# Optimization experiments

Hardware: AMD Instinct MI355X
Metric: run time of the kernel (lower is better)

The kernel has to match this reference:

```python
import jax, jax.numpy as jnp
import numpy as np

N, E, B, C, L, HLS = 30000, 480000, 64, 128, 3, 64
PARAM_NAMES = ['Wq','bq','Wk','bk','Wv','bv','Wskip','bskip','lstm_Wih_f','lstm_Whh_f','lstm_bih_f','lstm_bhh_f','lstm_Wih_b','lstm_Whh_b','lstm_bih_b','lstm_bhh_b','att_W','att_b','gP_W1','gP_b1','gP_W2','gP_b2','gT_W1','gT_b1','gT_W2','gT_b2','m_W0','m_b0','m_W1','m_b1','m_W2','m_b2']


def setup_inputs() -> dict:
    key = jax.random.key(0)
    ks = iter(jax.random.split(key, 64))
    rn = lambda shape: jax.random.normal(next(ks), shape, dtype=jnp.float32) * 0.05
    inp = {
        'x': jax.random.normal(next(ks), (N, C), dtype=jnp.float32),
        'edge_index': jax.random.randint(next(ks), (2, E), 0, N, dtype=jnp.int32),
        'batch': jnp.sort(jax.random.randint(next(ks), (N,), 0, B, dtype=jnp.int32)),
        'hls_attr': jax.random.normal(next(ks), (B, HLS), dtype=jnp.float32),
        'Wq': rn((L, C, C)), 'bq': rn((L, C)),
        'Wk': rn((L, C, C)), 'bk': rn((L, C)),
        'Wv': rn((L, C, C)), 'bv': rn((L, C)),
        'Wskip': rn((L, C, C)), 'bskip': rn((L, C)),
        'lstm_Wih_f': rn((4 * C, C)), 'lstm_Whh_f': rn((4 * C, C)),
        'lstm_bih_f': rn((4 * C,)), 'lstm_bhh_f': rn((4 * C,)),
        'lstm_Wih_b': rn((4 * C, C)), 'lstm_Whh_b': rn((4 * C, C)),
        'lstm_bih_b': rn((4 * C,)), 'lstm_bhh_b': rn((4 * C,)),
        'att_W': rn((2 * C, 1)), 'att_b': rn((1,)),
        'gP_W1': rn((C, C)), 'gP_b1': rn((C,)), 'gP_W2': rn((C, 1)), 'gP_b2': rn((1,)),
        'gT_W1': rn((C, C)), 'gT_b1': rn((C,)), 'gT_W2': rn((C, 1)), 'gT_b2': rn((1,)),
        'm_W0': rn((2 * C + HLS, 64)), 'm_b0': rn((64,)),
        'm_W1': rn((64, 64)), 'm_b1': rn((64,)),
        'm_W2': rn((64, 1)), 'm_b2': rn((1,)),
    }
    return inp


def _segment_softmax(logits, seg, num):
    m = jax.ops.segment_max(logits, seg, num_segments=num)
    e = jnp.exp(logits - m[seg])
    d = jax.ops.segment_sum(e, seg, num_segments=num)
    return e / d[seg]


def _lstm(xs, Wih, Whh, bih, bhh):
    # xs: [L, N, C] -> outputs [L, N, H]
    H = Whh.shape[1]
    h0 = jnp.zeros((xs.shape[1], H), xs.dtype)
    bias = bih + bhh
    def step(carry, xt):
        h, c = carry
        z = xt @ Wih.T + h @ Whh.T + bias
        i, f, g, o = jnp.split(z, 4, axis=-1)
        c = jax.nn.sigmoid(f) * c + jax.nn.sigmoid(i) * jnp.tanh(g)
        h = jax.nn.sigmoid(o) * jnp.tanh(c)
        return (h, c), h
    _, hs = jax.lax.scan(step, (h0, h0), xs)
    return hs


def _gate_pool(x, batch, W1, b1, W2, b2):
    gate = jax.nn.relu(x @ W1 + b1) @ W2 + b2          # [N, 1]
    gate = _segment_softmax(gate[:, 0], batch, B)[:, None]
    return jax.ops.segment_sum(gate * x, batch, num_segments=B)


def _forward(x, edge_index, batch, hls_attr, Wq, bq, Wk, bk, Wv, bv, Wskip, bskip,
             lstm_Wih_f, lstm_Whh_f, lstm_bih_f, lstm_bhh_f,
             lstm_Wih_b, lstm_Whh_b, lstm_bih_b, lstm_bhh_b,
             att_W, att_b, gP_W1, gP_b1, gP_W2, gP_b2, gT_W1, gT_b1, gT_W2, gT_b2,
             m_W0, m_b0, m_W1, m_b1, m_W2, m_b2):
    src, dst = edge_index[0], edge_index[1]
    scale = 1.0 / jnp.sqrt(jnp.asarray(C, jnp.float32))
    h_list = []
    for i in range(L):
        q = x @ Wq[i] + bq[i]
        k = x @ Wk[i] + bk[i]
        v = x @ Wv[i] + bv[i]
        logits = jnp.sum(q[dst] * k[src], axis=-1) * scale   # [E]
        alpha = _segment_softmax(logits, dst, N)             # per-dst softmax
        agg = jax.ops.segment_sum(alpha[:, None] * v[src], dst, num_segments=N)
        x = jax.nn.relu(agg + x @ Wskip[i] + bskip[i])       # TransformerConv + root skip, then ReLU
        h_list.append(x)
    xs = jnp.stack(h_list)                                   # [L, N, C]
    hf = _lstm(xs, lstm_Wih_f, lstm_Whh_f, lstm_bih_f, lstm_bhh_f)
    hb = _lstm(xs[::-1], lstm_Wih_b, lstm_Whh_b, lstm_bih_b, lstm_bhh_b)[::-1]
    hcat = jnp.concatenate([hf, hb], axis=-1)                # [L, N, 2C]
    a = jax.nn.softmax((hcat @ att_W)[..., 0] + att_b[0], axis=0)  # softmax over layers
    x = jnp.sum(a[..., None] * xs, axis=0)                   # [N, C] JK-LSTM output
    out_P = _gate_pool(x, batch, gP_W1, gP_b1, gP_W2, gP_b2)
    out_T = _gate_pool(x, batch, gT_W1, gT_b1, gT_W2, gT_b2)
    h = jnp.concatenate([out_P, out_T, hls_attr], axis=-1)   # [B, 2C+HLS]
    h = jax.nn.relu(h @ m_W0 + m_b0)
    h = jax.nn.relu(h @ m_W1 + m_b1)
    return h @ m_W2 + m_b2                                   # [B, 1]


def reference(x, edge_index, batch, hls_attr, Wq, bq, Wk, bk, Wv, bv, Wskip, bskip,
              lstm_Wih_f, lstm_Whh_f, lstm_bih_f, lstm_bhh_f,
              lstm_Wih_b, lstm_Whh_b, lstm_bih_b, lstm_bhh_b,
              att_W, att_b, gP_W1, gP_b1, gP_W2, gP_b2, gT_W1, gT_b1, gT_W2, gT_b2,
              m_W0, m_b0, m_W1, m_b1, m_W2, m_b2):
    return _forward(x, edge_index, batch, hls_attr, Wq, bq, Wk, bk, Wv, bv, Wskip, bskip,
                    lstm_Wih_f, lstm_Whh_f, lstm_bih_f, lstm_bhh_f,
                    lstm_Wih_b, lstm_Whh_b, lstm_bih_b, lstm_bhh_b,
                    att_W, att_b, gP_W1, gP_b1, gP_W2, gP_b2, gT_W1, gT_b1, gT_W2, gT_b2,
                    m_W0, m_b0, m_W1, m_b1, m_W2, m_b2)
```

## Files before the change

### kernel.cpp

```cpp
#include <hip/hip_runtime.h>
#include <math.h>

#define NN 30000
#define EE 480000
#define BB 64
#define CC 128
#define LLAYERS 3
#define HLSD 64

typedef __attribute__((ext_vector_type(8))) short bf16x8;
typedef __attribute__((ext_vector_type(4))) float f32x4;
typedef unsigned short u16;

__device__ inline unsigned short f2bf(float f){
  unsigned u = __float_as_uint(f);
  u += 0x7fffu + ((u >> 16) & 1u);
  return (unsigned short)(u >> 16);
}
__device__ inline float bf2f(unsigned short h){
  return __uint_as_float(((unsigned)h) << 16);
}
__device__ inline float fsig(float z){
  return __builtin_amdgcn_rcpf(1.f + __expf(-z));
}
__device__ inline float ftanh(float z){
  return 1.f - 2.f*__builtin_amdgcn_rcpf(1.f + __expf(2.f*z));
}

__global__ void k_hist(const int* __restrict__ dst, int* __restrict__ counts, int E){
  int e = blockIdx.x*256 + threadIdx.x;
  if (e < E) atomicAdd(&counts[dst[e]], 1);
}
__global__ void k_scan_block(const int* __restrict__ counts, int* __restrict__ row_ptr,
                             int* __restrict__ bsums, int n){
  __shared__ int sm[256];
  int i = blockIdx.x*256 + threadIdx.x;
  int v = (i < n) ? counts[i] : 0;
  sm[threadIdx.x] = v; __syncthreads();
  for (int off = 1; off < 256; off <<= 1){
    int t = (threadIdx.x >= off) ? sm[threadIdx.x - off] : 0;
    __syncthreads();
    sm[threadIdx.x] += t;
    __syncthreads();
  }
  if (i < n) row_ptr[i+1] = sm[threadIdx.x];
  if (threadIdx.x == 255) bsums[blockIdx.x] = sm[255];
}
__global__ void k_scan_bsums(const int* __restrict__ bsums, int* __restrict__ bexcl, int nb){
  if (threadIdx.x == 0 && blockIdx.x == 0){
    int s = 0;
    for (int i = 0; i < nb; i++){ int t = bsums[i]; bexcl[i] = s; s += t; }
  }
}
__global__ void k_scan_add(int* __restrict__ row_ptr, const int* __restrict__ bexcl, int n){
  int i = blockIdx.x*256 + threadIdx.x;
  if (i < n) row_ptr[i+1] += bexcl[i >> 8];
  if (i == 0) row_ptr[0] = 0;
}
__global__ void k_fill(const int* __restrict__ src, const int* __restrict__ dst,
                       const int* __restrict__ row_ptr, int* __restrict__ fill,
                       int* __restrict__ esrc, int E){
  int e = blockIdx.x*256 + threadIdx.x;
  if (e < E){
    int d = dst[e];
    int pos = row_ptr[d] + atomicAdd(&fill[d], 1);
    esrc[pos] = src[e];
  }
}

struct PrepPtrs {
  const float* tsrc[14]; unsigned short* tdst[14];
  const float* csrc[4];  unsigned short* cdst[4];
  const float *bihf, *bhhf, *bihb, *bhhb;
  float *cbf, *cbb;
};
__global__ __launch_bounds__(256) void k_prep(PrepPtrs p){
  int b = blockIdx.x, tid = threadIdx.x;
  if (b < 14){
    const float* s = p.tsrc[b]; unsigned short* d = p.tdst[b];
    for (int i = tid; i < 16384; i += 256){
      int k = i >> 7, n = i & 127;
      d[n*128 + k] = f2bf(s[i]);
    }
  } else if (b < 30){
    int m = (b - 14) >> 2, ch = (b - 14) & 3;
    const float* s = p.csrc[m] + ch*16384; unsigned short* d = p.cdst[m] + ch*16384;
    for (int i = tid; i < 16384; i += 256) d[i] = f2bf(s[i]);
  } else {
    for (int i = tid; i < 512; i += 256){
      p.cbf[i] = p.bihf[i] + p.bhhf[i];
      p.cbb[i] = p.bihb[i] + p.bhhb[i];
    }
  }
}
__global__ __launch_bounds__(256) void k_cvt_x(const float* __restrict__ src,
                                               unsigned short* __restrict__ dst, int n8){
  int i = blockIdx.x*256 + threadIdx.x;
  if (i >= n8) return;
  float4 a = *(const float4*)(src + (size_t)i*8);
  float4 b = *(const float4*)(src + (size_t)i*8 + 4);
  union { unsigned short u[8]; uint4 v; } o;
  o.u[0]=f2bf(a.x); o.u[1]=f2bf(a.y); o.u[2]=f2bf(a.z); o.u[3]=f2bf(a.w);
  o.u[4]=f2bf(b.x); o.u[5]=f2bf(b.y); o.u[6]=f2bf(b.z); o.u[7]=f2bf(b.w);
  *(uint4*)(dst + (size_t)i*8) = o.v;
}

struct Quad { const unsigned short* Bt[4]; const float* bias[4]; };

template<int RELU, int OUTBF16>
__global__ __launch_bounds__(256) void k_mfma_gemm(
    const unsigned short* __restrict__ A0, Quad qd,
    float* __restrict__ Cf, unsigned short* __restrict__ Cb,
    int M, int ldC, int colsPerMat)
{
  __shared__ unsigned short As0[64*128];
  __shared__ unsigned short Bs0[64*128];

  const int tid = threadIdx.x;
  const int row0 = blockIdx.x*64;
  const int colg0 = blockIdx.y*64;
  const int mi = colg0 / colsPerMat;
  const int nloc = colg0 - mi*colsPerMat;
  const unsigned short* Bt0 = qd.Bt[mi];

  #pragma unroll
  for (int i = 0; i < 4; i++){
    int ch = tid + i*256;
    int r = ch >> 4, c16 = ch & 15;
    int gr = row0 + r;
    uint4 av = make_uint4(0,0,0,0);
    if (gr < M) av = *(const uint4*)(A0 + (size_t)gr*128 + c16*8);
    *(uint4*)((char*)As0 + ((r*256 + c16*16) ^ ((r&7)<<4))) = av;
    uint4 bv = *(const uint4*)(Bt0 + (size_t)(nloc + r)*128 + c16*8);
    *(uint4*)((char*)Bs0 + ((r*256 + c16*16) ^ ((r&7)<<4))) = bv;
  }
  __syncthreads();

  const int w = tid >> 6, l = tid & 63;
  const int lr = l & 15, lhi = l >> 4;

  f32x4 acc[4];
  #pragma unroll
  for (int f = 0; f < 4; f++){ acc[f][0]=0.f; acc[f][1]=0.f; acc[f][2]=0.f; acc[f][3]=0.f; }

  #pragma unroll
  for (int kt = 0; kt < 4; kt++){
    int arow = w*16 + lr;
    bf16x8 a = *(const bf16x8*)((const char*)As0 + ((arow*256 + kt*64 + lhi*16) ^ ((arow&7)<<4)));
    #pragma unroll
    for (int f = 0; f < 4; f++){
      int brow = f*16 + lr;
      bf16x8 b = *(const bf16x8*)((const char*)Bs0 + ((brow*256 + kt*64 + lhi*16) ^ ((brow&7)<<4)));
      acc[f] = __builtin_amdgcn_mfma_f32_16x16x32_bf16(a, b, acc[f], 0, 0, 0);
    }
  }

  const float* bias = qd.bias[mi];
  #pragma unroll
  for (int f = 0; f < 4; f++){
    int colg = colg0 + f*16 + lr;
    float bv = bias ? bias[nloc + f*16 + lr] : 0.f;
    #pragma unroll
    for (int r = 0; r < 4; r++){
      int grow = row0 + w*16 + lhi*4 + r;
      if (grow < M){
        float v = acc[f][r] + bv;
        if (RELU) v = fmaxf(v, 0.f);
        if (OUTBF16) Cb[(size_t)grow*ldC + colg] = f2bf(v);
        else         Cf[(size_t)grow*ldC + colg] = v;
      }
    }
  }
}

struct LstmArgs {
  const u16 *Xf, *Xb, *Hf, *Hb;
  const u16 *Wihf, *Whhf, *Wihb, *Whhb;
  const float *cbf, *cbb;
  u16 *Hof, *Hob;
  float *Cf, *Cb2;
  float *scF, *scB;
  const float* attW;
  int M;
};
template<int FIRST>
__global__ __launch_bounds__(256) void k_lstm2(LstmArgs a){
  __shared__ unsigned short As[64*128];
  __shared__ unsigned short Bs[128*128];
  const int dir = blockIdx.y >> 2;
  const int t0 = (blockIdx.y & 3)*32;
  const u16* X = dir ? a.Xb : a.Xf;
  const u16* H = dir ? a.Hb : a.Hf;
  const u16* Wih = dir ? a.Wihb : a.Wihf;
  const u16* Whh = dir ? a.Whhb : a.Whhf;
  const float* cbias = dir ? a.cbb : a.cbf;
  u16* Hout = dir ? a.Hob : a.Hof;
  float* Cst = dir ? a.Cb2 : a.Cf;
  float* score = dir ? a.scB : a.scF;
  const float* attW = a.attW + dir*128;
  const int M = a.M;

  const int tid = threadIdx.x;
  const int row0 = blockIdx.x*64;
  const int w = tid >> 6, l = tid & 63, lr = l & 15, lhi = l >> 4;

  f32x4 acc[8];
  #pragma unroll
  for (int f = 0; f < 8; f++){ acc[f][0]=0.f; acc[f][1]=0.f; acc[f][2]=0.f; acc[f][3]=0.f; }

  const int npair = FIRST ? 1 : 2;
  for (int pair = 0; pair < npair; pair++){
    const unsigned short* A  = pair ? H   : X;
    const unsigned short* Bt = pair ? Whh : Wih;
    if (pair) __syncthreads();
    #pragma unroll
    for (int i = 0; i < 4; i++){
      int ch = tid + i*256;
      int r = ch >> 4, c16 = ch & 15;
      int gr = row0 + r;
      uint4 av = make_uint4(0,0,0,0);
      if (gr < M) av = *(const uint4*)(A + (size_t)gr*128 + c16*8);
      *(uint4*)((char*)As + ((r*256 + c16*16) ^ ((r&7)<<4))) = av;
    }
    #pragma unroll
    for (int i = 0; i < 8; i++){
      int ch = tid + i*256;
      int r = ch >> 4, c16 = ch & 15;
      int gr = (r >> 5)*128 + t0 + (r & 31);
      uint4 bv = *(const uint4*)(Bt + (size_t)gr*128 + c16*8);
      *(uint4*)((char*)Bs + ((r*256 + c16*16) ^ ((r&7)<<4))) = bv;
    }
    __syncthreads();
    #pragma unroll
    for (int kt = 0; kt < 4; kt++){
      int arow = w*16 + lr;
      bf16x8 av = *(const bf16x8*)((const char*)As + ((arow*256 + kt*64 + lhi*16) ^ ((arow&7)<<4)));
      #pragma unroll
      for (int f = 0; f < 8; f++){
        int brow = f*16 + lr;
        bf16x8 bv = *(const bf16x8*)((const char*)Bs + ((brow*256 + kt*64 + lhi*16) ^ ((brow&7)<<4)));
        acc[f] = __builtin_amdgcn_mfma_f32_16x16x32_bf16(av, bv, acc[f], 0, 0, 0);
      }
    }
  }

  float sc[4] = {0.f, 0.f, 0.f, 0.f};
  #pragma unroll
  for (int cb = 0; cb < 2; cb++){
    int t = t0 + cb*16 + lr;
    float aw  = attW[t];
    float bi  = cbias[t];
    float bf_ = cbias[128 + t];
    float bg  = cbias[256 + t];
    float bo  = cbias[384 + t];
    #pragma unroll
    for (int r = 0; r < 4; r++){
      int grow = row0 + w*16 + lhi*4 + r;
      if (grow < M){
        float zi = acc[0+cb][r] + bi;
        float zf = acc[2+cb][r] + bf_;
        float zg = acc[4+cb][r] + bg;
        float zo = acc[6+cb][r] + bo;
        float cp = FIRST ? 0.f : Cst[(size_t)grow*128 + t];
        float cn = fsig(zf)*cp + fsig(zi)*ftanh(zg);
        float hn = fsig(zo)*ftanh(cn);
        Cst[(size_t)grow*128 + t] = cn;
        Hout[(size_t)grow*128 + t] = f2bf(hn);
        sc[r] += hn * aw;
      }
    }
  }
  #pragma unroll
  for (int r = 0; r < 4; r++){
    float p = sc[r];
    p += __shfl_xor(p, 1, 64);
    p += __shfl_xor(p, 2, 64);
    p += __shfl_xor(p, 4, 64);
    p += __shfl_xor(p, 8, 64);
    if (lr == 0){
      int grow = row0 + w*16 + lhi*4 + r;
      if (grow < M) atomicAdd(&score[grow], p);
    }
  }
}

__global__ __launch_bounds__(256) void k_attn(
    const unsigned short* __restrict__ qkvs, const int* __restrict__ row_ptr,
    const int* __restrict__ esrc, unsigned short* __restrict__ xout, int n)
{
  int wid = threadIdx.x >> 6, lane = threadIdx.x & 63;
  int dst = blockIdx.x*4 + wid;
  if (dst >= n) return;
  const int g = lane >> 4, j = lane & 15;
  const size_t drow = (size_t)dst*512;

  bf16x8 qv = *(const bf16x8*)(qkvs + drow + j*8);
  float qf[8];
  #pragma unroll
  for (int i = 0; i < 8; i++) qf[i] = bf2f((unsigned short)qv[i]);

  const int rs = row_ptr[dst], re = row_ptr[dst+1];
  const float scale2 = 0.08838834764831845f * 1.4426950408889634f;
  float m = -INFINITY, den = 0.f;
  float acc[8];
  #pragma unroll
  for (int i = 0; i < 8; i++) acc[i] = 0.f;

  int e = rs + g;
  if (e < re){
    int s = esrc[e];
    const unsigned short* sr = qkvs + (size_t)s*512 + j*8;
    bf16x8 kc = *(const bf16x8*)(sr + 128);
    bf16x8 vc = *(const bf16x8*)(sr + 256);
    while (true){
      int en = e + 4;
      bool havenext = en < re;
      bf16x8 kn, vn;
      if (havenext){
        int sn = esrc[en];
        const unsigned short* srn = qkvs + (size_t)sn*512 + j*8;
        kn = *(const bf16x8*)(srn + 128);
        vn = *(const bf16x8*)(srn + 256);
      }
      float d = qf[0]*bf2f((unsigned short)kc[0]);
      #pragma unroll
      for (int i = 1; i < 8; i++) d += qf[i]*bf2f((unsigned short)kc[i]);
      d += __shfl_xor(d, 1, 64);
      d += __shfl_xor(d, 2, 64);
      d += __shfl_xor(d, 4, 64);
      d += __shfl_xor(d, 8, 64);
      float logit = d * scale2;
      float mn = fmaxf(m, logit);
      float rr = exp2f(m - mn);
      float wgt = exp2f(logit - mn);
      den = den*rr + wgt;
      #pragma unroll
      for (int i = 0; i < 8; i++)
        acc[i] = acc[i]*rr + wgt*bf2f((unsigned short)vc[i]);
      m = mn;
      if (!havenext) break;
      e = en; kc = kn; vc = vn;
    }
  }

  #pragma unroll
  for (int o = 16; o <= 32; o <<= 1){
    float mo  = __shfl_xor(m, o, 64);
    float dno = __shfl_xor(den, o, 64);
    float mn  = fmaxf(m, mo);
    float ss  = (m  > -INFINITY) ? exp2f(m  - mn) : 0.f;
    float so  = (mo > -INFINITY) ? exp2f(mo - mn) : 0.f;
    den = den*ss + dno*so;
    #pragma unroll
    for (int i = 0; i < 8; i++){
      float ao = __shfl_xor(acc[i], o, 64);
      acc[i] = acc[i]*ss + ao*so;
    }
    m = mn;
  }

  if (g == 0){
    bf16x8 sk = *(const bf16x8*)(qkvs + drow + 384 + j*8);
    float inv = (re > rs) ? 1.f/den : 0.f;
    union { unsigned short u[8]; uint4 v; } o8;
    #pragma unroll
    for (int i = 0; i < 8; i++){
      float v = acc[i]*inv + bf2f((unsigned short)sk[i]);
      o8.u[i] = f2bf(fmaxf(v, 0.f));
    }
    *(uint4*)(xout + (size_t)dst*128 + j*8) = o8.v;
  }
}

__global__ void k_jk_weights(const float* __restrict__ sF, const float* __restrict__ sB,
                             const float* __restrict__ attb, float* __restrict__ a, int n){
  int i = blockIdx.x*256 + threadIdx.x;
  if (i >= n) return;
  float s0 = sF[i]       + sB[i]       + attb[0];
  float s1 = sF[n+i]     + sB[n+i]     + attb[0];
  float s2 = sF[2*n+i]   + sB[2*n+i]   + attb[0];
  float mm = fmaxf(s0, fmaxf(s1, s2));
  float e0 = __expf(s0-mm), e1 = __expf(s1-mm), e2 = __expf(s2-mm);
  float d = e0 + e1 + e2;
  a[i] = e0/d; a[n+i] = e1/d; a[2*n+i] = e2/d;
}
__global__ void k_jk_combine(const float* __restrict__ a,
                             const unsigned short* __restrict__ x0,
                             const unsigned short* __restrict__ x1,
                             const unsigned short* __restrict__ x2,
                             float* __restrict__ xjk, unsigned short* __restrict__ xjkb, int n){
  int i8 = blockIdx.x*256 + threadIdx.x;
  if (i8 >= n*16) return;
  int node = i8 >> 4;
  float a0 = a[node], a1 = a[n+node], a2 = a[2*n+node];
  bf16x8 v0 = *(const bf16x8*)(x0 + (size_t)i8*8);
  bf16x8 v1 = *(const bf16x8*)(x1 + (size_t)i8*8);
  bf16x8 v2 = *(const bf16x8*)(x2 + (size_t)i8*8);
  float r[8];
  union { unsigned short u[8]; uint4 v; } ob;
  #pragma unroll
  for (int i = 0; i < 8; i++){
    r[i] = a0*bf2f((unsigned short)v0[i]) + a1*bf2f((unsigned short)v1[i]) + a2*bf2f((unsigned short)v2[i]);
    ob.u[i] = f2bf(r[i]);
  }
  float4* xo = (float4*)(xjk + (size_t)i8*8);
  xo[0] = make_float4(r[0], r[1], r[2], r[3]);
  xo[1] = make_float4(r[4], r[5], r[6], r[7]);
  *(uint4*)(xjkb + (size_t)i8*8) = ob.v;
}

__global__ __launch_bounds__(256) void k_rowdot2(
    const unsigned short* __restrict__ g,
    const float* __restrict__ w2P, const float* __restrict__ w2T,
    const float* __restrict__ b2P, const float* __restrict__ b2T,
    float* __restrict__ glP, float* __restrict__ glT, int n)
{
  int wid = threadIdx.x >> 6, lane = threadIdx.x & 63;
  int node = blockIdx.x*4 + wid;
  if (node >= n) return;
  ushort4 gv = *(const ushort4*)(g + (size_t)node*256 + lane*4);
  const float* w = (lane >= 32) ? w2T : w2P;
  int c0 = (lane*4) & 127;
  float4 wv = *(const float4*)(w + c0);
  float p = bf2f(gv.x)*wv.x + bf2f(gv.y)*wv.y + bf2f(gv.z)*wv.z + bf2f(gv.w)*wv.w;
  #pragma unroll
  for (int o = 1; o < 32; o <<= 1) p += __shfl_xor(p, o, 64);
  if (lane == 0)  glP[node] = p + b2P[0];
  if (lane == 32) glT[node] = p + b2T[0];
}

__global__ void k_segbounds(const int* __restrict__ batch, int* __restrict__ segp, int n){
  int i = blockIdx.x*256 + threadIdx.x;
  if (i >= n) return;
  int b = batch[i];
  int bp = (i == 0) ? -1 : batch[i-1];
  for (int s = bp+1; s <= b; s++) segp[s] = i;
  if (i == n-1){
    for (int s = b+1; s <= BB; s++) segp[s] = n;
  }
}

__global__ __launch_bounds__(256) void k_seg_stats(
    const float* __restrict__ glP, const float* __restrict__ glT,
    const int* __restrict__ segp, float4* __restrict__ stats)
{
  const int b = blockIdx.x, tid = threadIdx.x;
  const int s0 = segp[b], s1 = segp[b+1];
  __shared__ float sred[8];

  float mP = -INFINITY, mT = -INFINITY;
  for (int i = s0 + tid; i < s1; i += 256){
    mP = fmaxf(mP, glP[i]);
    mT = fmaxf(mT, glT[i]);
  }
  #pragma unroll
  for (int o = 1; o < 64; o <<= 1){
    mP = fmaxf(mP, __shfl_xor(mP, o, 64));
    mT = fmaxf(mT, __shfl_xor(mT, o, 64));
  }
  if ((tid & 63) == 0){ sred[(tid >> 6)*2] = mP; sred[(tid >> 6)*2 + 1] = mT; }
  __syncthreads();
  mP = fmaxf(fmaxf(sred[0], sred[2]), fmaxf(sred[4], sred[6]));
  mT = fmaxf(fmaxf(sred[1], sred[3]), fmaxf(sred[5], sred[7]));
  __syncthreads();

  float dP = 0.f, dT = 0.f;
  for (int i = s0 + tid; i < s1; i += 256){
    dP += __expf(glP[i] - mP);
    dT += __expf(glT[i] - mT);
  }
  #pragma unroll
  for (int o = 1; o < 64; o <<= 1){
    dP += __shfl_xor(dP, o, 64);
    dT += __shfl_xor(dT, o, 64);
  }
  if ((tid & 63) == 0){ sred[(tid >> 6)*2] = dP; sred[(tid >> 6)*2 + 1] = dT; }
  __syncthreads();
  if (tid == 0){
    dP = sred[0] + sred[2] + sred[4] + sred[6];
    dT = sred[1] + sred[3] + sred[5] + sred[7];
    float4 st;
    st.x = mP; st.y = mT;
    st.z = (dP > 0.f) ? 1.f/dP : 0.f;
    st.w = (dT > 0.f) ? 1.f/dT : 0.f;
    stats[b] = st;
  }
}

__global__ __launch_bounds__(256) void k_poolsum(
    const float* __restrict__ xjk, const int* __restrict__ segp,
    const float* __restrict__ glP, const float* __restrict__ glT,
    const float4* __restrict__ stats,
    float* __restrict__ poolP, float* __restrict__ poolT)
{
  const int b = blockIdx.x;
  const int s0 = segp[b], s1 = segp[b+1];
  const float4 st = stats[b];
  const int half = threadIdx.x >> 7, c = threadIdx.x & 127;
  const int stream = blockIdx.y*2 + half;
  float aP = 0.f, aT = 0.f;
  for (int i = s0 + stream; i < s1; i += 32){
    float eP = __expf(glP[i] - st.x);
    float eT = __expf(glT[i] - st.y);
    float xv = xjk[(size_t)i*128 + c];
    aP += eP*xv; aT += eT*xv;
  }
  if (aP != 0.f) atomicAdd(&poolP[(size_t)b*128 + c], aP*st.z);
  if (aT != 0.f) atomicAdd(&poolT[(size_t)b*128 + c], aT*st.w);
}

__global__ __launch_bounds__(64) void k_mlp(
    const float* __restrict__ poolP, const float* __restrict__ poolT, const float* __restrict__ hls,
    const float* __restrict__ W0, const float* __restrict__ b0,
    const float* __restrict__ W1, const float* __restrict__ b1,
    const float* __restrict__ W2, const float* __restrict__ b2, float* __restrict__ out)
{
  __shared__ float hin[320];
  __shared__ float h1[64];
  int b = blockIdx.x, j = threadIdx.x;
  for (int i = j; i < 320; i += 64){
    float vv;
    if (i < 128)      vv = poolP[(size_t)b*128 + i];
    else if (i < 256) vv = poolT[(size_t)b*128 + (i-128)];
    else              vv = hls[(size_t)b*64 + (i-256)];
    hin[i] = vv;
  }
  __syncthreads();
  float s = b0[j];
  for (int kk = 0; kk < 320; kk++) s += hin[kk] * W0[kk*64 + j];
  h1[j] = fmaxf(s, 0.f);
  __syncthreads();
  float s2 = b1[j];
  for (int kk = 0; kk < 64; kk++) s2 += h1[kk] * W1[kk*64 + j];
  float h2 = fmaxf(s2, 0.f);
  float p = h2 * W2[j];
  #pragma unroll
  for (int o = 1; o < 64; o <<= 1) p += __shfl_xor(p, o, 64);
  if (j == 0) out[b] = p + b2[0];
}

extern "C" void kernel_launch(void* const* d_in, const int* in_sizes, int n_in,
                              void* d_out, int out_size, void* d_ws, size_t ws_size,
                              hipStream_t stream)
{
  (void)in_sizes; (void)n_in; (void)out_size; (void)ws_size;
  const int N = NN, E = EE, C = CC;
  const float* x     = (const float*)d_in[0];
  const int*   ei    = (const int*)d_in[1];
  const int*   batch = (const int*)d_in[2];
  const float* hls   = (const float*)d_in[3];
  const float* Wq = (const float*)d_in[4],  *bq = (const float*)d_in[5];
  const float* Wk = (const float*)d_in[6],  *bk = (const float*)d_in[7];
  const float* Wv = (const float*)d_in[8],  *bv = (const float*)d_in[9];
  const float* Ws = (const float*)d_in[10], *bs = (const float*)d_in[11];
  const float* Wih_f = (const float*)d_in[12], *Whh_f = (const float*)d_in[13];
  const float* bih_f = (const float*)d_in[14], *bhh_f = (const float*)d_in[15];
  const float* Wih_b = (const float*)d_in[16], *Whh_b = (const float*)d_in[17];
  const float* bih_b = (const float*)d_in[18], *bhh_b = (const float*)d_in[19];
  const float* attW  = (const float*)d_in[20], *attb  = (const float*)d_in[21];
  const float* gPW1 = (const float*)d_in[22], *gPb1 = (const float*)d_in[23];
  const float* gPW2 = (const float*)d_in[24], *gPb2 = (const float*)d_in[25];
  const float* gTW1 = (const float*)d_in[26], *gTb1 = (const float*)d_in[27];
  const float* gTW2 = (const float*)d_in[28], *gTb2 = (const float*)d_in[29];
  const float* mW0 = (const float*)d_in[30], *mb0 = (const float*)d_in[31];
  const float* mW1 = (const float*)d_in[32], *mb1 = (const float*)d_in[33];
  const float* mW2 = (const float*)d_in[34], *mb2 = (const float*)d_in[35];
  float* out = (float*)d_out;

  const int* esrc_in = ei;
  const int* edst_in = ei + E;

  char* ws = (char*)d_ws;
  size_t off = 0;
  auto alloc = [&](size_t bytes) -> char* {
    char* p = ws + off;
    off += (bytes + 255) & ~(size_t)255;
    return p;
  };
  u16* qkvsb   = (u16*)alloc((size_t)N*512*2);
  u16* xb      = (u16*)alloc((size_t)N*C*2);
  u16* xsb0    = (u16*)alloc((size_t)N*C*2);
  u16* xsb1    = (u16*)alloc((size_t)N*C*2);
  u16* xsb2    = (u16*)alloc((size_t)N*C*2);
  u16* hfA     = (u16*)alloc((size_t)N*C*2);
  u16* hfB     = (u16*)alloc((size_t)N*C*2);
  u16* hbA     = (u16*)alloc((size_t)N*C*2);
  u16* hbB     = (u16*)alloc((size_t)N*C*2);
  float* cfb   = (float*)alloc((size_t)N*C*4);
  float* cbb2  = (float*)alloc((size_t)N*C*4);
  float* scores= (float*)alloc((size_t)6*N*4);
  float* ajk   = (float*)alloc((size_t)3*N*4);
  float* xjk   = (float*)alloc((size_t)N*C*4);
  u16* xjkb    = (u16*)alloc((size_t)N*C*2);
  u16* g1PT    = (u16*)alloc((size_t)N*256*2);
  int* counts  = (int*)alloc((size_t)N*4);
  int* row_ptr = (int*)alloc((size_t)(N+1)*4);
  int* bsums   = (int*)alloc(512);
  int* bexcl   = (int*)alloc(512);
  int* esrc    = (int*)alloc((size_t)E*4);
  float* glP   = (float*)alloc((size_t)N*4);
  float* glT   = (float*)alloc((size_t)N*4);
  int* segp    = (int*)alloc((size_t)(BB+1)*4);
  float* poolP = (float*)alloc((size_t)BB*C*4);
  float* poolT = (float*)alloc((size_t)BB*C*4);
  float4* sstats = (float4*)alloc((size_t)BB*16);
  u16* wT      = (u16*)alloc((size_t)14*16384*2);
  u16* wLSTM   = (u16*)alloc((size_t)4*65536*2);
  float* combF = (float*)alloc(512*4);
  float* combB = (float*)alloc(512*4);

  float* scF = scores;
  float* scB = scores + (size_t)3*N;

  u16* wTq = wT;
  u16* wTk = wT + 3*16384;
  u16* wTv = wT + 6*16384;
  u16* wTs = wT + 9*16384;
  u16* wTgP = wT + 12*16384;
  u16* wTgT = wT + 13*16384;
  u16* wIHf = wLSTM;
  u16* wHHf = wLSTM + 65536;
  u16* wIHb = wLSTM + 2*65536;
  u16* wHHb = wLSTM + 3*65536;

  const int NB  = (N + 255)/256;
  const int EBL = (E + 255)/256;

  PrepPtrs pp;
  for (int l = 0; l < 3; l++){
    pp.tsrc[l]   = Wq + (size_t)l*16384;  pp.tdst[l]   = wTq + (size_t)l*16384;
    pp.tsrc[3+l] = Wk + (size_t)l*16384;  pp.tdst[3+l] = wTk + (size_t)l*16384;
    pp.tsrc[6+l] = Wv + (size_t)l*16384;  pp.tdst[6+l] = wTv + (size_t)l*16384;
    pp.tsrc[9+l] = Ws + (size_t)l*16384;  pp.tdst[9+l] = wTs + (size_t)l*16384;
  }
  pp.tsrc[12] = gPW1; pp.tdst[12] = wTgP;
  pp.tsrc[13] = gTW1; pp.tdst[13] = wTgT;
  pp.csrc[0] = Wih_f; pp.cdst[0] = wIHf;
  pp.csrc[1] = Whh_f; pp.cdst[1] = wHHf;
  pp.csrc[2] = Wih_b; pp.cdst[2] = wIHb;
  pp.csrc[3] = Whh_b; pp.cdst[3] = wHHb;
  pp.bihf = bih_f; pp.bhhf = bhh_f; pp.bihb = bih_b; pp.bhhb = bhh_b;
  pp.cbf = combF; pp.cbb = combB;
  k_prep<<<31, 256, 0, stream>>>(pp);
  k_cvt_x<<<(N*C/8 + 255)/256, 256, 0, stream>>>(x, xb, N*C/8);

  hipMemsetAsync(counts, 0, (size_t)N*4, stream);
  k_hist<<<EBL, 256, 0, stream>>>(edst_in, counts, E);
  k_scan_block<<<NB, 256, 0, stream>>>(counts, row_ptr, bsums, N);
  k_scan_bsums<<<1, 64, 0, stream>>>(bsums, bexcl, NB);
  k_scan_add<<<NB, 256, 0, stream>>>(row_ptr, bexcl, N);
  hipMemsetAsync(counts, 0, (size_t)N*4, stream);
  k_fill<<<EBL, 256, 0, stream>>>(esrc_in, edst_in, row_ptr, counts, esrc, E);

  const int GX = (N + 63)/64;
  dim3 blk(256);

  u16* xsb[3] = {xsb0, xsb1, xsb2};
  const u16* ain = xb;
  for (int l = 0; l < LLAYERS; l++){
    Quad q;
    q.Bt[0] = wTq + (size_t)l*16384;  q.bias[0] = bq + (size_t)l*C;
    q.Bt[1] = wTk + (size_t)l*16384;  q.bias[1] = bk + (size_t)l*C;
    q.Bt[2] = wTv + (size_t)l*16384;  q.bias[2] = bv + (size_t)l*C;
    q.Bt[3] = wTs + (size_t)l*16384;  q.bias[3] = bs + (size_t)l*C;
    k_mfma_gemm<0,1><<<dim3(GX,8), blk, 0, stream>>>(ain, q, nullptr, qkvsb, N, 512, 128);
    k_attn<<<(N+3)/4, 256, 0, stream>>>(qkvsb, row_ptr, esrc, xsb[l], N);
    ain = xsb[l];
  }

  hipMemsetAsync(scores, 0, (size_t)6*N*4, stream);
  {
    u16* hfbuf[2] = {hfA, hfB};
    u16* hbbuf[2] = {hbA, hbB};
    for (int step = 0; step < 3; step++){
      LstmArgs la;
      la.Xf = xsb[step]; la.Xb = xsb[2-step];
      la.Hf = hfbuf[(step&1)^1]; la.Hb = hbbuf[(step&1)^1];
      la.Wihf = wIHf; la.Whhf = wHHf; la.Wihb = wIHb; la.Whhb = wHHb;
      la.cbf = combF; la.cbb = combB;
      la.Hof = hfbuf[step&1]; la.Hob = hbbuf[step&1];
      la.Cf = cfb; la.Cb2 = cbb2;
      la.scF = scF + (size_t)step*N; la.scB = scB + (size_t)(2-step)*N;
      la.attW = attW; la.M = N;
      if (step == 0) k_lstm2<1><<<dim3(GX,8), blk, 0, stream>>>(la);
      else           k_lstm2<0><<<dim3(GX,8), blk, 0, stream>>>(la);
    }
  }

  k_jk_weights<<<NB, 256, 0, stream>>>(scF, scB, attb, ajk, N);
  k_jk_combine<<<(N*16 + 255)/256, 256, 0, stream>>>(ajk, xsb0, xsb1, xsb2, xjk, xjkb, N);

  {
    Quad qg;
    qg.Bt[0] = wTgP; qg.bias[0] = gPb1;
    qg.Bt[1] = wTgT; qg.bias[1] = gTb1;
    qg.Bt[2] = nullptr; qg.bias[2] = nullptr;
    qg.Bt[3] = nullptr; qg.bias[3] = nullptr;
    k_mfma_gemm<1,1><<<dim3(GX,4), blk, 0, stream>>>(xjkb, qg, nullptr, g1PT, N, 256, 128);
    k_rowdot2<<<(N+3)/4, 256, 0, stream>>>(g1PT, gPW2, gTW2, gPb2, gTb2, glP, glT, N);
  }

  k_segbounds<<<NB, 256, 0, stream>>>(batch, segp, N);
  k_seg_stats<<<BB, 256, 0, stream>>>(glP, glT, segp, sstats);
  hipMemsetAsync(poolP, 0, (size_t)2*BB*C*4, stream);
  k_poolsum<<<dim3(BB,16), 256, 0, stream>>>(xjk, segp, glP, glT, sstats, poolP, poolT);

  k_mlp<<<BB, 64, 0, stream>>>(poolP, poolT, hls, mW0, mb0, mW1, mb1, mW2, mb2, out);
}
```

Before: 472.3 us.

## Fuse three bidirectional LSTM steps into one kernel with on-chip h/c state

The three per-step LSTM launches are replaced by a single kernel. Each block owns 64 rows and one direction, and it loops over all three timesteps and all four gate strips. Hidden state stays in LDS and cell state in registers, so the global H/C buffers, the score memset and the atomics are removed. In exchange, the grid shrinks from 8 to 2 blocks in y, which lowers parallelism. Weight tiles are also reloaded per strip per step with more syncs, and LDS use rises to about 80KB, which limits occupancy.

```diff
diff --git a/kernel.cpp b/kernel.cpp
--- a/kernel.cpp
+++ b/kernel.cpp
@@ -173,114 +173,147 @@
   }
 }
 
-struct LstmArgs {
-  const u16 *Xf, *Xb, *Hf, *Hb;
-  const u16 *Wihf, *Whhf, *Wihb, *Whhb;
-  const float *cbf, *cbb;
-  u16 *Hof, *Hob;
-  float *Cf, *Cb2;
-  float *scF, *scB;
-  const float* attW;
-  int M;
-};
-template<int FIRST>
-__global__ __launch_bounds__(256) void k_lstm2(LstmArgs a){
-  __shared__ unsigned short As[64*128];
-  __shared__ unsigned short Bs[128*128];
-  const int dir = blockIdx.y >> 2;
-  const int t0 = (blockIdx.y & 3)*32;
-  const u16* X = dir ? a.Xb : a.Xf;
-  const u16* H = dir ? a.Hb : a.Hf;
-  const u16* Wih = dir ? a.Wihb : a.Wihf;
-  const u16* Whh = dir ? a.Whhb : a.Whhf;
-  const float* cbias = dir ? a.cbb : a.cbf;
-  u16* Hout = dir ? a.Hob : a.Hof;
-  float* Cst = dir ? a.Cb2 : a.Cf;
-  float* score = dir ? a.scB : a.scF;
-  const float* attW = a.attW + dir*128;
-  const int M = a.M;
+__global__ __launch_bounds__(256) void k_lstm_all(
+    const u16* __restrict__ xsA, const u16* __restrict__ xsB, const u16* __restrict__ xsC,
+    const u16* __restrict__ WihF, const u16* __restrict__ WhhF,
+    const u16* __restrict__ WihB, const u16* __restrict__ WhhB,
+    const float* __restrict__ cbF, const float* __restrict__ cbB,
+    const float* __restrict__ attWall,
+    float* __restrict__ scF, float* __restrict__ scB, int M)
+{
+  __shared__ u16 Xs[64*128];
+  __shared__ u16 Hs[2][64*128];
+  __shared__ u16 Bs[128*128];
+
+  const int dir = blockIdx.y;
+  const u16* Wih = dir ? WihB : WihF;
+  const u16* Whh = dir ? WhhB : WhhF;
+  const float* cbias = dir ? cbB : cbF;
+  const float* attW = attWall + dir*128;
+  float* score = dir ? scB : scF;
+  const u16* xsrc[3];
+  xsrc[0] = dir ? xsC : xsA;
+  xsrc[1] = xsB;
+  xsrc[2] = dir ? xsA : xsC;
 
   const int tid = threadIdx.x;
   const int row0 = blockIdx.x*64;
   const int w = tid >> 6, l = tid & 63, lr = l & 15, lhi = l >> 4;
-
-  f32x4 acc[8];
-  #pragma unroll
-  for (int f = 0; f < 8; f++){ acc[f][0]=0.f; acc[f][1]=0.f; acc[f][2]=0.f; acc[f][3]=0.f; }
-
-  const int npair = FIRST ? 1 : 2;
-  for (int pair = 0; pair < npair; pair++){
-    const unsigned short* A  = pair ? H   : X;
-    const unsigned short* Bt = pair ? Whh : Wih;
-    if (pair) __syncthreads();
+  const int lrowbase = w*16 + lhi*4;
+
+  float cst[4][8];
+  #pragma unroll
+  for (int s = 0; s < 4; s++)
+    #pragma unroll
+    for (int i = 0; i < 8; i++) cst[s][i] = 0.f;
+
+  int cur = 0;
+  for (int t = 0; t < 3; t++){
+    const u16* X = xsrc[t];
+    __syncthreads();
     #pragma unroll
     for (int i = 0; i < 4; i++){
       int ch = tid + i*256;
       int r = ch >> 4, c16 = ch & 15;
       int gr = row0 + r;
       uint4 av = make_uint4(0,0,0,0);
-      if (gr < M) av = *(const uint4*)(A + (size_t)gr*128 + c16*8);
-      *(uint4*)((char*)As + ((r*256 + c16*16) ^ ((r&7)<<4))) = av;
-    }
+      if (gr < M) av = *(const uint4*)(X + (size_t)gr*128 + c16*8);
+      *(uint4*)((char*)Xs + ((r*256 + c16*16) ^ ((r&7)<<4))) = av;
+    }
+    u16* hwr = Hs[cur ^ 1];
+    const u16* hrd = Hs[cur];
+    float scacc[4] = {0.f, 0.f, 0.f, 0.f};
+
     #pragma unroll
-    for (int i = 0; i < 8; i++){
-      int ch = tid + i*256;
-      int r = ch >> 4, c16 = ch & 15;
-      int gr = (r >> 5)*128 + t0 + (r & 31);
-      uint4 bv = *(const uint4*)(Bt + (size_t)gr*128 + c16*8);
-      *(uint4*)((char*)Bs + ((r*256 + c16*16) ^ ((r&7)<<4))) = bv;
-    }
-    __syncthreads();
-    #pragma unroll
-    for (int kt = 0; kt < 4; kt++){
-      int arow = w*16 + lr;
-      bf16x8 av = *(const bf16x8*)((const char*)As + ((arow*256 + kt*64 + lhi*16) ^ ((arow&7)<<4)));
+    for (int strip = 0; strip < 4; strip++){
+      const int t0 = strip*32;
+      f32x4 acc[8];
       #pragma unroll
-      for (int f = 0; f < 8; f++){
-        int brow = f*16 + lr;
-        bf16x8 bv = *(const bf16x8*)((const char*)Bs + ((brow*256 + kt*64 + lhi*16) ^ ((brow&7)<<4)));
-        acc[f] = __builtin_amdgcn_mfma_f32_16x16x32_bf16(av, bv, acc[f], 0, 0, 0);
+      for (int f = 0; f < 8; f++){ acc[f][0]=0.f; acc[f][1]=0.f; acc[f][2]=0.f; acc[f][3]=0.f; }
+
+      #pragma unroll
+      for (int i = 0; i < 8; i++){
+        int ch = tid + i*256;
+        int r = ch >> 4, c16 = ch & 15;
+        int gr = (r >> 5)*128 + t0 + (r & 31);
+        uint4 bv = *(const uint4*)(Wih + (size_t)gr*128 + c16*8);
+        *(uint4*)((char*)Bs + ((r*256 + c16*16) ^ ((r&7)<<4))) = bv;
       }
-    }
-  }
-
-  float sc[4] = {0.f, 0.f, 0.f, 0.f};
-  #pragma unroll
-  for (int cb = 0; cb < 2; cb++){
-    int t = t0 + cb*16 + lr;
-    float aw  = attW[t];
-    float bi  = cbias[t];
-    float bf_ = cbias[128 + t];
-    float bg  = cbias[256 + t];
-    float bo  = cbias[384 + t];
+      __syncthreads();
+      #pragma unroll
+      for (int kt = 0; kt < 4; kt++){
+        int arow = w*16 + lr;
+        bf16x8 av = *(const bf16x8*)((const char*)Xs + ((arow*256 + kt*64 + lhi*16) ^ ((arow&7)<<4)));
+        #pragma unroll
+        for (int f = 0; f < 8; f++){
+          int brow = f*16 + lr;
+          bf16x8 bv = *(const bf16x8*)((const char*)Bs + ((brow*256 + kt*64 + lhi*16) ^ ((brow&7)<<4)));
+          acc[f] = __builtin_amdgcn_mfma_f32_16x16x32_bf16(av, bv, acc[f], 0, 0, 0);
+        }
+      }
+      if (t > 0){
+        __syncthreads();
+        #pragma unroll
+        for (int i = 0; i < 8; i++){
+          int ch = tid + i*256;
+          int r = ch >> 4, c16 = ch & 15;
+          int gr = (r >> 5)*128 + t0 + (r & 31);
+          uint4 bv = *(const uint4*)(Whh + (size_t)gr*128 + c16*8);
+          *(uint4*)((char*)Bs + ((r*256 + c16*16) ^ ((r&7)<<4))) = bv;
+        }
+        __syncthreads();
+        #pragma unroll
+        for (int kt = 0; kt < 4; kt++){
+          int arow = w*16 + lr;
+          bf16x8 av = *(const bf16x8*)((const char*)hrd + ((arow*256 + kt*64 + lhi*16) ^ ((arow&7)<<4)));
+          #pragma unroll
+          for (int f = 0; f < 8; f++){
+            int brow = f*16 + lr;
+            bf16x8 bv = *(const bf16x8*)((const char*)Bs + ((brow*256 + kt*64 + lhi*16) ^ ((brow&7)<<4)));
+            acc[f] = __builtin_amdgcn_mfma_f32_16x16x32_bf16(av, bv, acc[f], 0, 0, 0);
+          }
+        }
+      }
+      #pragma unroll
+      for (int cb = 0; cb < 2; cb++){
+        int ch = t0 + cb*16 + lr;
+        float aw  = attW[ch];
+        float bi  = cbias[ch];
+        float bf_ = cbias[128 + ch];
+        float bg  = cbias[256 + ch];
+        float bo  = cbias[384 + ch];
+        #pragma unroll
+        for (int r = 0; r < 4; r++){
+          float zi = acc[0+cb][r] + bi;
+          float zf = acc[2+cb][r] + bf_;
+          float zg = acc[4+cb][r] + bg;
+          float zo = acc[6+cb][r] + bo;
+          float cp = cst[strip][cb*4+r];
+          float cn = fsig(zf)*cp + fsig(zi)*ftanh(zg);
+          float hn = fsig(zo)*ftanh(cn);
+          cst[strip][cb*4+r] = cn;
+          int lrow = lrowbase + r;
+          *(u16*)((char*)hwr + ((lrow*256 + ch*2) ^ ((lrow&7)<<4))) = f2bf(hn);
+          scacc[r] += hn * aw;
+        }
+      }
+      __syncthreads();
+    }
+
+    const int soff = (dir ? (2 - t) : t) * M;
     #pragma unroll
     for (int r = 0; r < 4; r++){
-      int grow = row0 + w*16 + lhi*4 + r;
-      if (grow < M){
-        float zi = acc[0+cb][r] + bi;
-        float zf = acc[2+cb][r] + bf_;
-        float zg = acc[4+cb][r] + bg;
-        float zo = acc[6+cb][r] + bo;
-        float cp = FIRST ? 0.f : Cst[(size_t)grow*128 + t];
-        float cn = fsig(zf)*cp + fsig(zi)*ftanh(zg);
-        float hn = fsig(zo)*ftanh(cn);
-        Cst[(size_t)grow*128 + t] = cn;
-        Hout[(size_t)grow*128 + t] = f2bf(hn);
-        sc[r] += hn * aw;
+      float p = scacc[r];
+      p += __shfl_xor(p, 1, 64);
+      p += __shfl_xor(p, 2, 64);
+      p += __shfl_xor(p, 4, 64);
+      p += __shfl_xor(p, 8, 64);
+      if (lr == 0){
+        int grow = row0 + lrowbase + r;
+        if (grow < M) score[soff + grow] = p;
       }
     }
-  }
-  #pragma unroll
-  for (int r = 0; r < 4; r++){
-    float p = sc[r];
-    p += __shfl_xor(p, 1, 64);
-    p += __shfl_xor(p, 2, 64);
-    p += __shfl_xor(p, 4, 64);
-    p += __shfl_xor(p, 8, 64);
-    if (lr == 0){
-      int grow = row0 + w*16 + lhi*4 + r;
-      if (grow < M) atomicAdd(&score[grow], p);
-    }
+    cur ^= 1;
   }
 }
 
@@ -582,12 +615,6 @@
   u16* xsb0    = (u16*)alloc((size_t)N*C*2);
   u16* xsb1    = (u16*)alloc((size_t)N*C*2);
   u16* xsb2    = (u16*)alloc((size_t)N*C*2);
-  u16* hfA     = (u16*)alloc((size_t)N*C*2);
-  u16* hfB     = (u16*)alloc((size_t)N*C*2);
-  u16* hbA     = (u16*)alloc((size_t)N*C*2);
-  u16* hbB     = (u16*)alloc((size_t)N*C*2);
-  float* cfb   = (float*)alloc((size_t)N*C*4);
-  float* cbb2  = (float*)alloc((size_t)N*C*4);
   float* scores= (float*)alloc((size_t)6*N*4);
   float* ajk   = (float*)alloc((size_t)3*N*4);
   float* xjk   = (float*)alloc((size_t)N*C*4);
@@ -668,24 +695,8 @@
     ain = xsb[l];
   }
 
-  hipMemsetAsync(scores, 0, (size_t)6*N*4, stream);
-  {
-    u16* hfbuf[2] = {hfA, hfB};
-    u16* hbbuf[2] = {hbA, hbB};
-    for (int step = 0; step < 3; step++){
-      LstmArgs la;
-      la.Xf = xsb[step]; la.Xb = xsb[2-step];
-      la.Hf = hfbuf[(step&1)^1]; la.Hb = hbbuf[(step&1)^1];
-      la.Wihf = wIHf; la.Whhf = wHHf; la.Wihb = wIHb; la.Whhb = wHHb;
-      la.cbf = combF; la.cbb = combB;
-      la.Hof = hfbuf[step&1]; la.Hob = hbbuf[step&1];
-      la.Cf = cfb; la.Cb2 = cbb2;
-      la.scF = scF + (size_t)step*N; la.scB = scB + (size_t)(2-step)*N;
-      la.attW = attW; la.M = N;
-      if (step == 0) k_lstm2<1><<<dim3(GX,8), blk, 0, stream>>>(la);
-      else           k_lstm2<0><<<dim3(GX,8), blk, 0, stream>>>(la);
-    }
-  }
+  k_lstm_all<<<dim3(GX,2), blk, 0, stream>>>(xsb0, xsb1, xsb2, wIHf, wHHf, wIHb, wHHb,
+                                             combF, combB, attW, scF, scB, N);
 
   k_jk_weights<<<NB, 256, 0, stream>>>(scF, scB, attb, ajk, N);
   k_jk_combine<<<(N*16 + 255)/256, 256, 0, stream>>>(ajk, xsb0, xsb1, xsb2, xjk, xjkb, N);
```

After: 507.2 us. 1.07x slower.
